# Optimization experiments

Hardware: AMD Instinct MI355X
Metric: run time of the kernel (lower is better)

Reference implementation:

```python
import jax, jax.numpy as jnp
import numpy as np

EPS_AGG = 1e-6  # torch code adds 1e-6 to scatter weight sums
EPS_BN = 1e-5


def _pix_idx(loc_orig, H, W):
    # map normalized coords in [-1,1] to flat pixel index on an HxW grid
    loc = jnp.clip(loc_orig, -1.0, 1.0) * 0.5 + 0.5
    ix = jnp.round(loc[..., 0] * (W - 1)).astype(jnp.int32)
    iy = jnp.round(loc[..., 1] * (H - 1)).astype(jnp.int32)
    return iy * W + ix  # [B, N0]


def token2map(x, loc_orig, idx_agg, H, W):
    # scatter token features to a dense map, averaging collisions
    B, N, C = x.shape
    N0 = idx_agg.shape[1]
    idx_hw = _pix_idx(loc_orig, H, W)                                   # [B, N0]
    tok = jnp.take_along_axis(x, idx_agg[..., None], axis=1)            # [B, N0, C]
    flat = (idx_hw + jnp.arange(B, dtype=jnp.int32)[:, None] * (H * W)).reshape(-1)
    sums = jax.ops.segment_sum(tok.reshape(-1, C), flat, num_segments=B * H * W)
    cnt = jax.ops.segment_sum(jnp.ones((B * N0,), x.dtype), flat, num_segments=B * H * W)
    out = sums / (cnt[:, None] + EPS_AGG)
    return out.reshape(B, H, W, C).transpose(0, 3, 1, 2)                # [B, C, H, W]


def map2token(fmap, Nt, loc_orig, idx_agg_t, agg_weight_t):
    # gather map pixels back to Nt target tokens, weighted-averaging per token
    B, C, H, W = fmap.shape
    idx_hw = _pix_idx(loc_orig, H, W)                                   # [B, N0]
    pix = fmap.transpose(0, 2, 3, 1).reshape(B, H * W, C)
    gath = jnp.take_along_axis(pix, idx_hw[..., None], axis=1)          # [B, N0, C]
    flat = (idx_agg_t + jnp.arange(B, dtype=jnp.int32)[:, None] * Nt).reshape(-1)
    num = jax.ops.segment_sum((gath * agg_weight_t[..., None]).reshape(-1, C), flat, num_segments=B * Nt)
    den = jax.ops.segment_sum(agg_weight_t.reshape(-1), flat, num_segments=B * Nt)
    return (num / (den[:, None] + EPS_AGG)).reshape(B, Nt, C)


def token_downup(x, idx_agg_s, idx_agg_t, agg_weight_t, Nt):
    # weighted aggregation from N source tokens to Nt target tokens via N0 original positions
    B, N, C = x.shape
    src = jnp.take_along_axis(x, idx_agg_s[..., None], axis=1)          # [B, N0, C]
    flat = (idx_agg_t + jnp.arange(B, dtype=jnp.int32)[:, None] * Nt).reshape(-1)
    num = jax.ops.segment_sum((src * agg_weight_t[..., None]).reshape(-1, C), flat, num_segments=B * Nt)
    den = jax.ops.segment_sum(agg_weight_t.reshape(-1), flat, num_segments=B * Nt)
    return (num / (den[:, None] + EPS_AGG)).reshape(B, Nt, C)


def batchnorm(x, gamma, beta):
    # BatchNorm2d on [B,C,Nt,1] == per-channel stats over (B, Nt); x here is [B, Nt, C]
    mu = x.mean(axis=(0, 1), keepdims=True)
    var = x.var(axis=(0, 1), keepdims=True)
    return (x - mu) * jax.lax.rsqrt(var + EPS_BN) * gamma + beta


def setup_inputs() -> dict:
    key = jax.random.key(0)
    ks = jax.random.split(key, 12)
    B, N, N0, Nt, Cin, Cout, H, W = 32, 1568, 3136, 784, 256, 512, 56, 56
    x = jax.random.normal(ks[0], (B, N, Cin), dtype=jnp.float32)
    loc_orig = jax.random.uniform(ks[1], (B, N0, 2), dtype=jnp.float32, minval=-1.0, maxval=1.0)
    idx_agg = jax.random.randint(ks[2], (B, N0), 0, N, dtype=jnp.int32)
    agg_weight = jax.random.uniform(ks[3], (B, N0), dtype=jnp.float32)
    idx_agg_t = jax.random.randint(ks[4], (B, N0), 0, Nt, dtype=jnp.int32)
    agg_weight_t = jax.random.uniform(ks[5], (B, N0), dtype=jnp.float32)
    dw_w = jax.random.normal(ks[6], (Cin, 1, 3, 3), dtype=jnp.float32) * 0.1     # depthwise 3x3
    skip_w = jax.random.normal(ks[7], (Cin,), dtype=jnp.float32) * 0.1           # depthwise 1x1
    conv_w = jax.random.normal(ks[8], (Cout, Cin), dtype=jnp.float32) * (1.0 / np.sqrt(Cin))
    gamma1 = jnp.ones((Cin,), jnp.float32); beta1 = jnp.zeros((Cin,), jnp.float32)
    gamma2 = jnp.ones((Cout,), jnp.float32); beta2 = jnp.zeros((Cout,), jnp.float32)
    return {"x": x, "loc_orig": loc_orig, "idx_agg": idx_agg, "agg_weight": agg_weight,
            "idx_agg_t": idx_agg_t, "agg_weight_t": agg_weight_t, "H": H, "W": W, "Nt": Nt,
            "dw_w": dw_w, "skip_w": skip_w, "conv_w": conv_w,
            "gamma1": gamma1, "beta1": beta1, "gamma2": gamma2, "beta2": beta2}


def reference(x, loc_orig, idx_agg, agg_weight, idx_agg_t, agg_weight_t, H, W, Nt,
              dw_w, skip_w, conv_w, gamma1, beta1, gamma2, beta2):
    # token -> map scatter
    x_map = token2map(x, loc_orig, idx_agg, H, W)                       # [B, Cin, H, W]
    # 3x3 depthwise conv, stride 2, padding 1
    Cin = x_map.shape[1]
    x_map = jax.lax.conv_general_dilated(
        x_map, dw_w, window_strides=(2, 2), padding=((1, 1), (1, 1)),
        feature_group_count=Cin, dimension_numbers=("NCHW", "OIHW", "NCHW"))    # [B, Cin, H/2, W/2]
    # map -> target tokens gather
    x_back = map2token(x_map, Nt, loc_orig, idx_agg_t, agg_weight_t)    # [B, Nt, Cin]
    # skip path: token downsample + 1x1 depthwise (per-channel scale)
    xs = token_downup(x, idx_agg, idx_agg_t, agg_weight_t, Nt)          # [B, Nt, Cin]
    xs = xs * skip_w                                                    # dw_skip, groups=Cin, k=1
    y = xs + x_back
    y = batchnorm(y, gamma1, beta1)
    y = jnp.einsum("bnc,oc->bno", y, conv_w)                            # 1x1 conv Cin->Cout
    y = batchnorm(y, gamma2, beta2)
    return jax.nn.relu(y)                                               # [B, Nt, Cout]
```

## Files before the change

### kernel.cpp

```cpp
#include <hip/hip_runtime.h>

constexpr int B    = 32;
constexpr int N    = 1568;
constexpr int N0   = 3136;
constexpr int Nt   = 784;
constexpr int Cin  = 256;
constexpr int Cout = 512;
constexpr int H    = 56;
constexpr int W    = 56;
constexpr int HW   = 3136;
constexpr int Ho   = 28;
constexpr int Wo   = 28;
constexpr int HWo  = 784;
constexpr int RR   = B * Nt;
constexpr int NE   = B * N0;
constexpr int NBP  = B * HW;
constexpr int NBT  = B * Nt;
constexpr int NBO  = B * HWo;
constexpr int SB   = NBT + NBO;
constexpr int NCHUNK = SB / 256;

constexpr size_t W_HISTP = 0;
constexpr size_t W_HISTS = NBP;
constexpr size_t W_S1SUM = NBP + SB;
constexpr size_t W_S1SQ  = W_S1SUM + Cin;
constexpr size_t W_S2SUM = W_S1SQ + Cin;
constexpr size_t W_S2SQ  = W_S2SUM + Cout;
constexpr size_t W_OFF   = NBP + SB + 1536;
constexpr size_t W_CUR   = W_OFF + SB + 8;
constexpr size_t W_PC    = W_CUR + SB;
constexpr size_t W_BSUM  = W_PC + NE;
constexpr size_t W_LT    = W_BSUM + 512;
constexpr size_t W_LC    = W_LT + (size_t)2 * NE;
constexpr size_t W_CONVB = W_LC + (size_t)8 * NE;
constexpr size_t W_YBF   = W_CONVB + (size_t)B * HWo * Cin / 2;
constexpr size_t W_WFB   = W_YBF + (size_t)RR * Cin / 2;
constexpr size_t W_BIAS  = W_WFB + (size_t)Cout * Cin / 2;
constexpr size_t W_ZB    = W_BIAS + Cout;

__device__ __forceinline__ int pix_of(float t, float scale) {
    t = fminf(fmaxf(t, -1.0f), 1.0f);
    float u = __fadd_rn(__fmul_rn(t, 0.5f), 0.5f);
    return (int)rintf(__fmul_rn(u, scale));
}
__device__ __forceinline__ unsigned short f2bf(float f) {
    unsigned int u = __float_as_uint(f);
    u = (u + 0x7fffu + ((u >> 16) & 1u)) >> 16;
    return (unsigned short)u;
}
__device__ __forceinline__ float bf2f(unsigned short h) {
    return __uint_as_float(((unsigned int)h) << 16);
}

__global__ void k_hist(const float* __restrict__ loc, const int* __restrict__ idxt,
                       int* __restrict__ histP, int* __restrict__ histS,
                       int* __restrict__ pc) {
    int i = blockIdx.x * 256 + threadIdx.x;
    if (i >= NE) return;
    int b = i / N0;
    float lx = loc[(size_t)2 * i], ly = loc[(size_t)2 * i + 1];
    int ix = pix_of(lx, 55.0f), iy = pix_of(ly, 55.0f);
    int jx = pix_of(lx, 27.0f), jy = pix_of(ly, 27.0f);
    int p56 = iy * W + ix, p28 = jy * Wo + jx;
    pc[i] = p56 | (p28 << 16);
    atomicAdd(&histP[b * HW + p56], 1);
    atomicAdd(&histS[b * Nt + idxt[i]], 1);
    int oy_lo = iy >> 1, oy_hi = min(Ho - 1, (iy + 1) >> 1);
    int ox_lo = ix >> 1, ox_hi = min(Wo - 1, (ix + 1) >> 1);
    for (int oy = oy_lo; oy <= oy_hi; ++oy)
        for (int ox = ox_lo; ox <= ox_hi; ++ox)
            atomicAdd(&histS[NBT + b * HWo + oy * Wo + ox], 1);
}

__global__ void k_scanA(const int* __restrict__ hist, int* __restrict__ bsum) {
    __shared__ int sm[256];
    int i = blockIdx.x * 256 + threadIdx.x;
    sm[threadIdx.x] = hist[i];
    __syncthreads();
    for (int d = 128; d > 0; d >>= 1) {
        if (threadIdx.x < d) sm[threadIdx.x] += sm[threadIdx.x + d];
        __syncthreads();
    }
    if (threadIdx.x == 0) bsum[blockIdx.x] = sm[0];
}

__global__ void k_scanB(int* __restrict__ bsum) {
    __shared__ int sm[512];
    int t = threadIdx.x;
    int v = (t < NCHUNK) ? bsum[t] : 0;
    sm[t] = v; __syncthreads();
    for (int d = 1; d < 512; d <<= 1) {
        int u = (t >= d) ? sm[t - d] : 0;
        __syncthreads();
        sm[t] += u;
        __syncthreads();
    }
    if (t < NCHUNK) bsum[t] = sm[t] - v;
}

__global__ void k_scanC(const int* __restrict__ hist, const int* __restrict__ bsum,
                        int* __restrict__ off, int* __restrict__ cur) {
    __shared__ int sm[256];
    int t = threadIdx.x;
    int i = blockIdx.x * 256 + t;
    int v = hist[i];
    sm[t] = v; __syncthreads();
    for (int d = 1; d < 256; d <<= 1) {
        int u = (t >= d) ? sm[t - d] : 0;
        __syncthreads();
        sm[t] += u;
        __syncthreads();
    }
    int excl = bsum[blockIdx.x] + sm[t] - v;
    off[i] = excl; cur[i] = excl;
    if (i == SB - 1) off[SB] = excl + v;
}

__global__ void k_scat(const int* __restrict__ pc, const int* __restrict__ idxa,
                       const int* __restrict__ idxt, const float* __restrict__ wt,
                       const int* __restrict__ histP, int* __restrict__ cur,
                       int2* __restrict__ listT, int2* __restrict__ listC) {
    int i = blockIdx.x * 256 + threadIdx.x;
    if (i >= NE) return;
    int b = i / N0;
    int v = pc[i];
    int p56 = v & 0xFFFF, p28 = v >> 16;
    int s = idxa[i];
    int posT = atomicAdd(&cur[b * Nt + idxt[i]], 1);
    listT[posT] = make_int2(s | (p28 << 16), __float_as_int(wt[i]));
    float wrc = 1.0f / ((float)histP[b * HW + p56] + 1e-6f);
    int wrci = __float_as_int(wrc);
    int iy = p56 / W, ix = p56 - iy * W;
    int oy_lo = iy >> 1, oy_hi = min(Ho - 1, (iy + 1) >> 1);
    int ox_lo = ix >> 1, ox_hi = min(Wo - 1, (ix + 1) >> 1);
    for (int oy = oy_lo; oy <= oy_hi; ++oy)
        for (int ox = ox_lo; ox <= ox_hi; ++ox) {
            int tap = (iy - (2 * oy - 1)) * 3 + (ix - (2 * ox - 1));
            int posC = atomicAdd(&cur[NBT + b * HWo + oy * Wo + ox], 1) - NE;
            listC[posC] = make_int2(s | (tap << 16), wrci);
        }
}

__global__ __launch_bounds__(256) void k_gconv(const float* __restrict__ x,
        const int* __restrict__ off, const int2* __restrict__ listC,
        const float* __restrict__ dww, unsigned short* __restrict__ convb) {
    __shared__ float wsm[9 * 256];
    int t = threadIdx.x;
#pragma unroll
    for (int k = 0; k < 9; ++k) wsm[k * 256 + t] = dww[t * 9 + k];
    int wv = t >> 6, lane = t & 63;
    int blk = blockIdx.x * 4 + wv;
    int b   = __builtin_amdgcn_readfirstlane(blk / HWo);
    int st  = __builtin_amdgcn_readfirstlane(off[NBT + blk]) - NE;
    int en  = __builtin_amdgcn_readfirstlane(off[NBT + blk + 1]) - NE;
    __syncthreads();
    const float* xb = x + (size_t)b * N * Cin;
    float4 acc = make_float4(0.f, 0.f, 0.f, 0.f);
    int j = st;
    for (; j + 4 <= en; j += 4) {
        int2 e0 = listC[j], e1 = listC[j + 1], e2 = listC[j + 2], e3 = listC[j + 3];
        float4 v0 = ((const float4*)(xb + (size_t)(e0.x & 0xFFFF) * Cin))[lane];
        float4 v1 = ((const float4*)(xb + (size_t)(e1.x & 0xFFFF) * Cin))[lane];
        float4 v2 = ((const float4*)(xb + (size_t)(e2.x & 0xFFFF) * Cin))[lane];
        float4 v3 = ((const float4*)(xb + (size_t)(e3.x & 0xFFFF) * Cin))[lane];
        float4 w0 = *(const float4*)&wsm[(e0.x >> 16) * 256 + lane * 4];
        float4 w1 = *(const float4*)&wsm[(e1.x >> 16) * 256 + lane * 4];
        float4 w2 = *(const float4*)&wsm[(e2.x >> 16) * 256 + lane * 4];
        float4 w3 = *(const float4*)&wsm[(e3.x >> 16) * 256 + lane * 4];
        float r0 = __int_as_float(e0.y), r1 = __int_as_float(e1.y);
        float r2 = __int_as_float(e2.y), r3 = __int_as_float(e3.y);
        acc.x = fmaf(v0.x * r0, w0.x, acc.x);
        acc.y = fmaf(v0.y * r0, w0.y, acc.y);
        acc.z = fmaf(v0.z * r0, w0.z, acc.z);
        acc.w = fmaf(v0.w * r0, w0.w, acc.w);
        acc.x = fmaf(v1.x * r1, w1.x, acc.x);
        acc.y = fmaf(v1.y * r1, w1.y, acc.y);
        acc.z = fmaf(v1.z * r1, w1.z, acc.z);
        acc.w = fmaf(v1.w * r1, w1.w, acc.w);
        acc.x = fmaf(v2.x * r2, w2.x, acc.x);
        acc.y = fmaf(v2.y * r2, w2.y, acc.y);
        acc.z = fmaf(v2.z * r2, w2.z, acc.z);
        acc.w = fmaf(v2.w * r2, w2.w, acc.w);
        acc.x = fmaf(v3.x * r3, w3.x, acc.x);
        acc.y = fmaf(v3.y * r3, w3.y, acc.y);
        acc.z = fmaf(v3.z * r3, w3.z, acc.z);
        acc.w = fmaf(v3.w * r3, w3.w, acc.w);
    }
    for (; j < en; ++j) {
        int2 e = listC[j];
        float4 v = ((const float4*)(xb + (size_t)(e.x & 0xFFFF) * Cin))[lane];
        float4 wq = *(const float4*)&wsm[(e.x >> 16) * 256 + lane * 4];
        float r = __int_as_float(e.y);
        acc.x = fmaf(v.x * r, wq.x, acc.x);
        acc.y = fmaf(v.y * r, wq.y, acc.y);
        acc.z = fmaf(v.z * r, wq.z, acc.z);
        acc.w = fmaf(v.w * r, wq.w, acc.w);
    }
    uint2 o;
    o.x = (unsigned int)f2bf(acc.x) | ((unsigned int)f2bf(acc.y) << 16);
    o.y = (unsigned int)f2bf(acc.z) | ((unsigned int)f2bf(acc.w) << 16);
    ((uint2*)(convb + (size_t)blk * Cin))[lane] = o;
}

__global__ __launch_bounds__(256) void k_gtok(const float* __restrict__ x,
        const unsigned short* __restrict__ convb, const int* __restrict__ off,
        const int2* __restrict__ listT, const float* __restrict__ skipw,
        unsigned short* __restrict__ ybf) {
    int t = threadIdx.x, wv = t >> 6, lane = t & 63;
    int bt = blockIdx.x * 4 + wv;
    int b  = __builtin_amdgcn_readfirstlane(bt / Nt);
    int st = __builtin_amdgcn_readfirstlane(off[bt]);
    int en = __builtin_amdgcn_readfirstlane(off[bt + 1]);
    const float* xb = x + (size_t)b * N * Cin;
    const unsigned short* cbb = convb + (size_t)b * HWo * Cin;
    float4 sk = ((const float4*)skipw)[lane];
    float4 acc = make_float4(0.f, 0.f, 0.f, 0.f);
    float wsum = 0.0f;
    int j = st;
    for (; j + 2 <= en; j += 2) {
        int2 e0 = listT[j], e1 = listT[j + 1];
        float4 xv0 = ((const float4*)(xb + (size_t)(e0.x & 0xFFFF) * Cin))[lane];
        float4 xv1 = ((const float4*)(xb + (size_t)(e1.x & 0xFFFF) * Cin))[lane];
        uint2 cv0 = ((const uint2*)(cbb + (size_t)(e0.x >> 16) * Cin))[lane];
        uint2 cv1 = ((const uint2*)(cbb + (size_t)(e1.x >> 16) * Cin))[lane];
        float w0 = __int_as_float(e0.y), w1 = __int_as_float(e1.y);
        wsum += w0 + w1;
        acc.x = fmaf(w0, bf2f((unsigned short)(cv0.x & 0xffffu)) + sk.x * xv0.x, acc.x);
        acc.y = fmaf(w0, bf2f((unsigned short)(cv0.x >> 16))     + sk.y * xv0.y, acc.y);
        acc.z = fmaf(w0, bf2f((unsigned short)(cv0.y & 0xffffu)) + sk.z * xv0.z, acc.z);
        acc.w = fmaf(w0, bf2f((unsigned short)(cv0.y >> 16))     + sk.w * xv0.w, acc.w);
        acc.x = fmaf(w1, bf2f((unsigned short)(cv1.x & 0xffffu)) + sk.x * xv1.x, acc.x);
        acc.y = fmaf(w1, bf2f((unsigned short)(cv1.x >> 16))     + sk.y * xv1.y, acc.y);
        acc.z = fmaf(w1, bf2f((unsigned short)(cv1.y & 0xffffu)) + sk.z * xv1.z, acc.z);
        acc.w = fmaf(w1, bf2f((unsigned short)(cv1.y >> 16))     + sk.w * xv1.w, acc.w);
    }
    for (; j < en; ++j) {
        int2 e = listT[j];
        float4 xv = ((const float4*)(xb + (size_t)(e.x & 0xFFFF) * Cin))[lane];
        uint2 cv = ((const uint2*)(cbb + (size_t)(e.x >> 16) * Cin))[lane];
        float w = __int_as_float(e.y);
        wsum += w;
        acc.x = fmaf(w, bf2f((unsigned short)(cv.x & 0xffffu)) + sk.x * xv.x, acc.x);
        acc.y = fmaf(w, bf2f((unsigned short)(cv.x >> 16))     + sk.y * xv.y, acc.y);
        acc.z = fmaf(w, bf2f((unsigned short)(cv.y & 0xffffu)) + sk.z * xv.z, acc.z);
        acc.w = fmaf(w, bf2f((unsigned short)(cv.y >> 16))     + sk.w * xv.w, acc.w);
    }
    float rw = 1.0f / (wsum + 1e-6f);
    uint2 o;
    o.x = (unsigned int)f2bf(acc.x * rw) | ((unsigned int)f2bf(acc.y * rw) << 16);
    o.y = (unsigned int)f2bf(acc.z * rw) | ((unsigned int)f2bf(acc.w * rw) << 16);
    ((uint2*)(ybf + (size_t)bt * Cin))[lane] = o;
}

__global__ void k_ystats(const unsigned short* __restrict__ ybf,
                         float* __restrict__ s1, float* __restrict__ s1q) {
    int t = threadIdx.x;
    int half = t >> 7, ci = t & 127;
    float sum0 = 0.f, sq0 = 0.f, sum1 = 0.f, sq1 = 0.f;
    for (int r = blockIdx.x * 2 + half; r < RR; r += gridDim.x * 2) {
        unsigned int u = ((const unsigned int*)(ybf + (size_t)r * Cin))[ci];
        float v0 = bf2f((unsigned short)(u & 0xffffu));
        float v1 = bf2f((unsigned short)(u >> 16));
        sum0 += v0; sq0 = fmaf(v0, v0, sq0);
        sum1 += v1; sq1 = fmaf(v1, v1, sq1);
    }
    atomicAdd(&s1[ci * 2],      sum0);
    atomicAdd(&s1q[ci * 2],     sq0);
    atomicAdd(&s1[ci * 2 + 1],  sum1);
    atomicAdd(&s1q[ci * 2 + 1], sq1);
}

__global__ void k_fold(const float* __restrict__ s1, const float* __restrict__ s1q,
                       const float* __restrict__ g1, const float* __restrict__ b1,
                       const float* __restrict__ convw, unsigned short* __restrict__ wfb,
                       float* __restrict__ bias) {
    int o = blockIdx.x, c = threadIdx.x;
    const float inv = 1.0f / (float)RR;
    float mu  = s1[c] * inv;
    float var = s1q[c] * inv - mu * mu;
    float a   = g1[c] / sqrtf(var + 1e-5f);
    float bs  = b1[c] - mu * a;
    float wv  = convw[(size_t)o * Cin + c];
    wfb[(size_t)o * Cin + c] = f2bf(wv * a);
    __shared__ float red[256];
    red[c] = wv * bs;
    __syncthreads();
    for (int st = 128; st > 0; st >>= 1) {
        if (c < st) red[c] += red[c + st];
        __syncthreads();
    }
    if (c == 0) bias[o] = red[0];
}

typedef __attribute__((ext_vector_type(8))) short short8;
typedef __attribute__((ext_vector_type(4))) float f32x4;

__global__ __launch_bounds__(256) void k_gemm(const unsigned short* __restrict__ A,
        const unsigned short* __restrict__ Bt, const float* __restrict__ bias,
        unsigned short* __restrict__ zb, float* __restrict__ s2, float* __restrict__ s2q) {
    constexpr int BK = 32, LS = 48;
    __shared__ unsigned short As[128 * LS];
    __shared__ unsigned short Bs[128 * LS];
    __shared__ float rsum[128], rsq[128];
    int m0 = blockIdx.x * 128, n0 = blockIdx.y * 128;
    int t = threadIdx.x;
    int wave = t >> 6, lane = t & 63;
    int wm = wave >> 1, wn = wave & 1;
    int l16 = lane & 15, lq = lane >> 4;
    f32x4 acc[4][4];
#pragma unroll
    for (int i = 0; i < 4; ++i)
#pragma unroll
        for (int j = 0; j < 4; ++j) acc[i][j] = (f32x4)0.0f;
    if (t < 128) { rsum[t] = 0.0f; rsq[t] = 0.0f; }

    for (int k0 = 0; k0 < Cin; k0 += BK) {
#pragma unroll
        for (int r2 = 0; r2 < 2; ++r2) {
            int e = r2 * 256 + t;
            int row = e >> 2, kc = (e & 3) * 8;
            *(float4*)&As[row * LS + kc] = *(const float4*)&A[((size_t)(m0 + row)) * Cin + k0 + kc];
            *(float4*)&Bs[row * LS + kc] = *(const float4*)&Bt[((size_t)(n0 + row)) * Cin + k0 + kc];
        }
        __syncthreads();
        short8 af[4], bf[4];
#pragma unroll
        for (int i = 0; i < 4; ++i) {
            af[i] = *(short8*)&As[(wm * 64 + i * 16 + l16) * LS + lq * 8];
            bf[i] = *(short8*)&Bs[(wn * 64 + i * 16 + l16) * LS + lq * 8];
        }
#pragma unroll
        for (int i = 0; i < 4; ++i)
#pragma unroll
            for (int j = 0; j < 4; ++j)
                acc[i][j] = __builtin_amdgcn_mfma_f32_16x16x32_bf16(af[i], bf[j], acc[i][j], 0, 0, 0);
        __syncthreads();
    }
#pragma unroll
    for (int j = 0; j < 4; ++j) {
        int cl  = wn * 64 + j * 16 + l16;
        int col = n0 + cl;
        float bv = bias[col];
        float ps = 0.0f, pq = 0.0f;
#pragma unroll
        for (int i = 0; i < 4; ++i) {
            int rbase = m0 + wm * 64 + i * 16 + lq * 4;
#pragma unroll
            for (int r = 0; r < 4; ++r) {
                float v = acc[i][j][r] + bv;
                zb[(size_t)(rbase + r) * Cout + col] = f2bf(v);
                ps += v;
                pq = fmaf(v, v, pq);
            }
        }
        atomicAdd(&rsum[cl], ps);
        atomicAdd(&rsq[cl], pq);
    }
    __syncthreads();
    if (t < 128) {
        atomicAdd(&s2[n0 + t], rsum[t]);
        atomicAdd(&s2q[n0 + t], rsq[t]);
    }
}

__global__ void k_final(const unsigned short* __restrict__ zb,
                        const float* __restrict__ s2, const float* __restrict__ s2q,
                        const float* __restrict__ g2, const float* __restrict__ b2,
                        float* __restrict__ out) {
    size_t j4 = ((size_t)blockIdx.x * 256 + threadIdx.x) * 4;
    int o = (int)(j4 & (Cout - 1));
    const float inv = 1.0f / (float)RR;
    uint2 u = *(const uint2*)&zb[j4];
    float e0 = bf2f((unsigned short)(u.x & 0xffffu));
    float e1 = bf2f((unsigned short)(u.x >> 16));
    float e2 = bf2f((unsigned short)(u.y & 0xffffu));
    float e3 = bf2f((unsigned short)(u.y >> 16));
    float mu0 = s2[o + 0] * inv, a0 = g2[o + 0] * rsqrtf(s2q[o + 0] * inv - mu0 * mu0 + 1e-5f);
    float mu1 = s2[o + 1] * inv, a1 = g2[o + 1] * rsqrtf(s2q[o + 1] * inv - mu1 * mu1 + 1e-5f);
    float mu2 = s2[o + 2] * inv, a2 = g2[o + 2] * rsqrtf(s2q[o + 2] * inv - mu2 * mu2 + 1e-5f);
    float mu3 = s2[o + 3] * inv, a3 = g2[o + 3] * rsqrtf(s2q[o + 3] * inv - mu3 * mu3 + 1e-5f);
    float c0 = b2[o + 0] - mu0 * a0;
    float c1 = b2[o + 1] - mu1 * a1;
    float c2 = b2[o + 2] - mu2 * a2;
    float c3 = b2[o + 3] - mu3 * a3;
    float4 r;
    r.x = fmaxf(fmaf(e0, a0, c0), 0.0f);
    r.y = fmaxf(fmaf(e1, a1, c1), 0.0f);
    r.z = fmaxf(fmaf(e2, a2, c2), 0.0f);
    r.w = fmaxf(fmaf(e3, a3, c3), 0.0f);
    *(float4*)&out[j4] = r;
}

extern "C" void kernel_launch(void* const* d_in, const int* in_sizes, int n_in,
                              void* d_out, int out_size, void* d_ws, size_t ws_size,
                              hipStream_t stream) {
    const float* x     = (const float*)d_in[0];
    const float* loc   = (const float*)d_in[1];
    const int*   idxa  = (const int*)d_in[2];
    const int*   idxt  = (const int*)d_in[4];
    const float* wt    = (const float*)d_in[5];
    const float* dww   = (const float*)d_in[9];
    const float* skipw = (const float*)d_in[10];
    const float* convw = (const float*)d_in[11];
    const float* g1    = (const float*)d_in[12];
    const float* b1    = (const float*)d_in[13];
    const float* g2    = (const float*)d_in[14];
    const float* b2    = (const float*)d_in[15];

    float* ws = (float*)d_ws;
    int*   histP = (int*)(ws + W_HISTP);
    int*   histS = (int*)(ws + W_HISTS);
    float* s1sum = ws + W_S1SUM;
    float* s1sq  = ws + W_S1SQ;
    float* s2sum = ws + W_S2SUM;
    float* s2sq  = ws + W_S2SQ;
    int*   off   = (int*)(ws + W_OFF);
    int*   cur   = (int*)(ws + W_CUR);
    int*   pc    = (int*)(ws + W_PC);
    int*   bsum  = (int*)(ws + W_BSUM);
    int2*  listT = (int2*)(ws + W_LT);
    int2*  listC = (int2*)(ws + W_LC);
    unsigned short* convb = (unsigned short*)(ws + W_CONVB);
    unsigned short* ybf   = (unsigned short*)(ws + W_YBF);
    unsigned short* wfb   = (unsigned short*)(ws + W_WFB);
    float* bias  = ws + W_BIAS;
    unsigned short* zb = (unsigned short*)(ws + W_ZB);
    float* out   = (float*)d_out;

    hipMemsetAsync(histP, 0, (size_t)(NBP + SB + 1536) * sizeof(float), stream);

    k_hist<<<NE / 256, 256, 0, stream>>>(loc, idxt, histP, histS, pc);
    k_scanA<<<NCHUNK, 256, 0, stream>>>(histS, bsum);
    k_scanB<<<1, 512, 0, stream>>>(bsum);
    k_scanC<<<NCHUNK, 256, 0, stream>>>(histS, bsum, off, cur);
    k_scat<<<NE / 256, 256, 0, stream>>>(pc, idxa, idxt, wt, histP, cur, listT, listC);

    k_gconv<<<NBO / 4, 256, 0, stream>>>(x, off, listC, dww, convb);
    k_gtok<<<NBT / 4, 256, 0, stream>>>(x, convb, off, listT, skipw, ybf);
    k_ystats<<<256, 256, 0, stream>>>(ybf, s1sum, s1sq);
    k_fold<<<Cout, 256, 0, stream>>>(s1sum, s1sq, g1, b1, convw, wfb, bias);

    dim3 gg(RR / 128, Cout / 128);
    k_gemm<<<gg, 256, 0, stream>>>(ybf, wfb, bias, zb, s2sum, s2sq);
    k_final<<<(int)(((size_t)RR * Cout) / 1024), 256, 0, stream>>>(zb, s2sum, s2sq, g2, b2, out);
}
```

Measured before the change: 287.7 us.

## Load full-K GEMM tiles into LDS via global_load_lds with XOR swizzle

The bf16 GEMM kernel now stages the whole K=256 extent of both 128-row tiles into LDS up front using direct global-to-LDS loads, and uses an XOR-swizzled layout in place of padded rows. This removes the per-K-step barrier loop and register round-trip for tile staging, and the swizzle is meant to avoid LDS bank conflicts on the fragment reads. In exchange each block uses about 128KB of LDS and is limited to one block per CU, so load latency is no longer overlapped with compute from other blocks. The GEMM is only one of several kernels in the pipeline.

```diff
diff --git a/kernel.cpp b/kernel.cpp
--- a/kernel.cpp
+++ b/kernel.cpp
@@ -50,6 +50,11 @@
 }
 __device__ __forceinline__ float bf2f(unsigned short h) {
     return __uint_as_float(((unsigned int)h) << 16);
+}
+__device__ __forceinline__ void gload_lds16(const void* g, void* lds) {
+    __builtin_amdgcn_global_load_lds(
+        (const __attribute__((address_space(1))) void*)g,
+        (__attribute__((address_space(3))) void*)lds, 16, 0, 0);
 }
 
 __global__ void k_hist(const float* __restrict__ loc, const int* __restrict__ idxt,
@@ -295,47 +300,68 @@
 typedef __attribute__((ext_vector_type(8))) short short8;
 typedef __attribute__((ext_vector_type(4))) float f32x4;
 
-__global__ __launch_bounds__(256) void k_gemm(const unsigned short* __restrict__ A,
+__global__ __launch_bounds__(256, 1) void k_gemm(const unsigned short* __restrict__ A,
         const unsigned short* __restrict__ Bt, const float* __restrict__ bias,
         unsigned short* __restrict__ zb, float* __restrict__ s2, float* __restrict__ s2q) {
-    constexpr int BK = 32, LS = 48;
-    __shared__ unsigned short As[128 * LS];
-    __shared__ unsigned short Bs[128 * LS];
+    __shared__ unsigned short As[128 * 256];
+    __shared__ unsigned short Bs[128 * 256];
     __shared__ float rsum[128], rsq[128];
     int m0 = blockIdx.x * 128, n0 = blockIdx.y * 128;
     int t = threadIdx.x;
     int wave = t >> 6, lane = t & 63;
     int wm = wave >> 1, wn = wave & 1;
     int l16 = lane & 15, lq = lane >> 4;
+    if (t < 128) { rsum[t] = 0.0f; rsq[t] = 0.0f; }
+
+    {
+        int rlo = lane >> 5;
+        int ch  = lane & 31;
+#pragma unroll
+        for (int p = 0; p < 16; ++p) {
+            int row = wave * 32 + p * 2 + rlo;
+            int sc  = ch ^ (row & 7);
+            gload_lds16(A + (size_t)(m0 + row) * Cin + sc * 8,
+                        &As[(wave * 32 + p * 2) * 256]);
+        }
+#pragma unroll
+        for (int p = 0; p < 16; ++p) {
+            int row = wave * 32 + p * 2 + rlo;
+            int sc  = ch ^ (row & 7);
+            gload_lds16(Bt + (size_t)(n0 + row) * Cin + sc * 8,
+                        &Bs[(wave * 32 + p * 2) * 256]);
+        }
+    }
+    asm volatile("s_waitcnt vmcnt(0)" ::: "memory");
+    __syncthreads();
+
     f32x4 acc[4][4];
 #pragma unroll
     for (int i = 0; i < 4; ++i)
 #pragma unroll
         for (int j = 0; j < 4; ++j) acc[i][j] = (f32x4)0.0f;
-    if (t < 128) { rsum[t] = 0.0f; rsq[t] = 0.0f; }
-
-    for (int k0 = 0; k0 < Cin; k0 += BK) {
-#pragma unroll
-        for (int r2 = 0; r2 < 2; ++r2) {
-            int e = r2 * 256 + t;
-            int row = e >> 2, kc = (e & 3) * 8;
-            *(float4*)&As[row * LS + kc] = *(const float4*)&A[((size_t)(m0 + row)) * Cin + k0 + kc];
-            *(float4*)&Bs[row * LS + kc] = *(const float4*)&Bt[((size_t)(n0 + row)) * Cin + k0 + kc];
-        }
-        __syncthreads();
+
+#pragma unroll
+    for (int ks = 0; ks < 8; ++ks) {
         short8 af[4], bf[4];
 #pragma unroll
         for (int i = 0; i < 4; ++i) {
-            af[i] = *(short8*)&As[(wm * 64 + i * 16 + l16) * LS + lq * 8];
-            bf[i] = *(short8*)&Bs[(wn * 64 + i * 16 + l16) * LS + lq * 8];
+            int row = wm * 64 + i * 16 + l16;
+            int c   = (ks * 4 + lq) ^ (row & 7);
+            af[i] = *(short8*)&As[row * 256 + c * 8];
+        }
+#pragma unroll
+        for (int j = 0; j < 4; ++j) {
+            int row = wn * 64 + j * 16 + l16;
+            int c   = (ks * 4 + lq) ^ (row & 7);
+            bf[j] = *(short8*)&Bs[row * 256 + c * 8];
         }
 #pragma unroll
         for (int i = 0; i < 4; ++i)
 #pragma unroll
             for (int j = 0; j < 4; ++j)
                 acc[i][j] = __builtin_amdgcn_mfma_f32_16x16x32_bf16(af[i], bf[j], acc[i][j], 0, 0, 0);
-        __syncthreads();
-    }
+    }
+
 #pragma unroll
     for (int j = 0; j < 4; ++j) {
         int cl  = wn * 64 + j * 16 + l16;
```

Result: no change. 285.6 us (-0.7%).
